# Performance work log

Measured on AMD Instinct MI355X. Metric: run time of the kernel, lower is better.

## Reference

```python
import jax, jax.numpy as jnp
import numpy as np

N = 500000
TOL = 0.01
ALPHA = 0.1
SLOPE = 0.01
EPS = 1e-10


def smooth_relu(x):
    # 0 for x<0; x^2/2 for 0<=x<1; x-1/2 for x>=1 (C1 smooth ReLU)
    return jnp.where(x < 0, 0.0, jnp.where(x < 1, 0.5 * x * x, x - 0.5))


def leaky_relu(x):
    return jnp.where(x >= 0, x, SLOPE * x)


def _xavier(key, shape):
    fan_out, fan_in = shape
    std = np.sqrt(2.0 / (fan_in + fan_out)).astype(np.float32)
    return jax.random.normal(key, shape, dtype=jnp.float32) * std


def setup_inputs() -> dict:
    key = jax.random.key(0)
    ks = jax.random.split(key, 16)
    inp = {
        'X': jax.random.normal(ks[0], (N, 2), dtype=jnp.float32),
        'Xstable': jnp.zeros((N, 2), dtype=jnp.float32),
        'Vl1_w': _xavier(ks[1], (64, 2)),
        'V2x_w': _xavier(ks[2], (64, 2)),
        'V2z_w': _xavier(ks[3], (64, 64)),
        'V3x_w': _xavier(ks[4], (64, 2)),
        'V3z_w': _xavier(ks[5], (64, 64)),
        'Vfx_w': _xavier(ks[6], (1, 2)),
        'Vfz_w': _xavier(ks[7], (1, 64)),
        'f1_w': _xavier(ks[8], (128, 2)),
        'f1_b': jnp.zeros((128,), dtype=jnp.float32),
        'f2_w': _xavier(ks[9], (128, 128)),
        'f2_b': jnp.zeros((128,), dtype=jnp.float32),
        'f3_w': _xavier(ks[10], (128, 128)),
        'f3_b': jnp.zeros((128,), dtype=jnp.float32),
        'f4_w': _xavier(ks[11], (128, 128)),
        'f4_b': jnp.zeros((128,), dtype=jnp.float32),
        'f5_w': _xavier(ks[12], (128, 128)),
        'f5_b': jnp.zeros((128,), dtype=jnp.float32),
        'ff_w': _xavier(ks[13], (2, 128)),
        'ff_b': jnp.zeros((2,), dtype=jnp.float32),
    }
    return inp


def _V_forward(X, Xstable, Vl1_w, V2x_w, V2z_w, V3x_w, V3z_w, Vfx_w, Vfz_w):
    d = X - Xstable                                  # [N,2]
    z1 = smooth_relu(d @ Vl1_w.T)                    # [N,64]
    z2 = smooth_relu(d @ V2x_w.T + z1 @ V2z_w.T)     # [N,64]
    z3 = smooth_relu(d @ V3x_w.T + z2 @ V3z_w.T)     # [N,64]
    zf = smooth_relu(d @ Vfx_w.T + z3 @ Vfz_w.T)     # [N,1]
    vsum = TOL * jnp.sum(d * d, axis=1, keepdims=True)
    return smooth_relu(zf) + vsum                    # [N,1]


def _fhat_forward(X, f1_w, f1_b, f2_w, f2_b, f3_w, f3_b, f4_w, f4_b, f5_w, f5_b, ff_w, ff_b):
    h = leaky_relu(X @ f1_w.T + f1_b)
    h = leaky_relu(h @ f2_w.T + f2_b)
    h = leaky_relu(h @ f3_w.T + f3_b)
    h = leaky_relu(h @ f4_w.T + f4_b)
    h = leaky_relu(h @ f5_w.T + f5_b)
    return h @ ff_w.T + ff_b                         # [N,2]


def reference(X, Xstable, Vl1_w, V2x_w, V2z_w, V3x_w, V3z_w, Vfx_w, Vfz_w,
              f1_w, f1_b, f2_w, f2_b, f3_w, f3_b, f4_w, f4_b, f5_w, f5_b, ff_w, ff_b):
    def Vfn(Xv):
        return _V_forward(Xv, Xstable, Vl1_w, V2x_w, V2z_w, V3x_w, V3z_w, Vfx_w, Vfz_w)

    V, pullback = jax.vjp(Vfn, X)
    gradV = pullback(jnp.ones_like(V))[0]            # dV/dX, [N,2]

    f_hat = _fhat_forward(X, f1_w, f1_b, f2_w, f2_b, f3_w, f3_b,
                          f4_w, f4_b, f5_w, f5_b, ff_w, ff_b)

    Vnorm = jnp.sum(gradV * gradV, axis=1, keepdims=True)      # [N,1]
    fh_V = jnp.sum(f_hat * gradV, axis=1, keepdims=True)       # [N,1]
    f_mul = jax.nn.relu(fh_V + ALPHA * V) / (Vnorm + EPS)      # [N,1]
    f = f_hat - gradV * f_mul                                  # [N,2]
    return f
```

## Files before the change

### kernel.cpp

```cpp
#include <hip/hip_runtime.h>


typedef _Float16 v2h __attribute__((ext_vector_type(2)));
typedef __fp16   v2hf __attribute__((ext_vector_type(2)));
typedef _Float16 v4h __attribute__((ext_vector_type(4)));
typedef _Float16 v8h __attribute__((ext_vector_type(8)));
typedef float    v4f __attribute__((ext_vector_type(4)));

__device__ __forceinline__ v2h cvt_pk(float a, float b){
  v2hf r = __builtin_amdgcn_cvt_pkrtz(a, b);
  union { v2hf f; v2h h; } u; u.f = r;
  return u.h;
}

#define NPTS 500000
#define FUSED_GRID ((NPTS + 255) / 256)

#define BAR_LDS() asm volatile("s_waitcnt lgkmcnt(0)\n\ts_barrier" ::: "memory")

#define OFF_FW    0
#define OFF_V2Z   65536
#define OFF_V3Z   69632
#define OFF_V2ZT  73728
#define OFF_V3ZT  77824
#define OFF_VL1T  81920
#define OFF_V2XT  82048
#define OFF_V3XT  82176
#define OFF_VFZ   82304
#define OFF_FFW   82368
#define OFF_F1W   82624
#define OFF_F1P   82880
#define OFF_V2XP  86976
#define OFF_V3XP  89024
#define W16_DATA  91072
#define W16_TOTAL (W16_DATA + 2048)

__device__ __align__(16) _Float16 g_w16[W16_TOTAL];

__device__ __forceinline__ float srelu(float x){
  float c = fminf(fmaxf(x, 0.f), 1.f);
  return c * fmaf(-0.5f, c, x);
}
__device__ __forceinline__ float sreluD(float x){
  return fminf(fmaxf(x, 0.f), 1.f);
}
__device__ __forceinline__ float sreluD_from_z(float z){
  return fminf(sqrtf(2.f * z), 1.f);
}

__device__ __forceinline__ v2h lrelu_pk(float a, float b){
  v2h x = cvt_pk(a, b);
  v2h m = x * (v2h){(_Float16)0.01f, (_Float16)0.01f};
  return __builtin_elementwise_max(x, m);
}
__device__ __forceinline__ v2h srelu_pk(float a, float b){
  v2h x = cvt_pk(a, b);
  const v2h z0 = (v2h){(_Float16)0.f, (_Float16)0.f};
  const v2h o1 = (v2h){(_Float16)1.f, (_Float16)1.f};
  const v2h hf = (v2h){(_Float16)0.5f, (_Float16)0.5f};
  v2h c = __builtin_elementwise_min(__builtin_elementwise_max(x, z0), o1);
  v2h t = x - c * hf;
  return c * t;
}

__global__ __launch_bounds__(256) void prep_kernel(
  const float* __restrict__ f2w, const float* __restrict__ f3w,
  const float* __restrict__ f4w, const float* __restrict__ f5w,
  const float* __restrict__ V2z, const float* __restrict__ V3z,
  const float* __restrict__ Vl1, const float* __restrict__ V2x,
  const float* __restrict__ V3x, const float* __restrict__ Vfz,
  const float* __restrict__ ffw, const float* __restrict__ f1w)
{
  const int i = blockIdx.x * 256 + threadIdx.x;
  if (i >= W16_TOTAL) return;
  if (i >= W16_DATA){ g_w16[i] = (_Float16)0.f; return; }
  float v;
  if (i < 65536){
    const float* W[4] = {f2w, f3w, f4w, f5w};
    v = W[i >> 14][i & 16383];
  } else if (i < 69632)  v = V2z[i - 65536];
  else if (i < 73728)    v = V3z[i - 69632];
  else if (i < 77824){ int r = i - 73728; v = V2z[(r & 63)*64 + (r >> 6)]; }
  else if (i < 81920){ int r = i - 77824; v = V3z[(r & 63)*64 + (r >> 6)]; }
  else if (i < 82048){ int r = i - 81920; v = Vl1[(r & 63)*2 + (r >> 6)]; }
  else if (i < 82176){ int r = i - 82048; v = V2x[(r & 63)*2 + (r >> 6)]; }
  else if (i < 82304){ int r = i - 82176; v = V3x[(r & 63)*2 + (r >> 6)]; }
  else if (i < 82368)    v = Vfz[i - 82304];
  else if (i < 82624)    v = ffw[i - 82368];
  else if (i < 82880)    v = f1w[i - 82624];
  else if (i < 86976){ int r = i - 82880; int k = r & 31; v = (k < 2) ? f1w[(r >> 5)*2 + k] : 0.f; }
  else if (i < 89024){ int r = i - 86976; int k = r & 31; v = (k < 2) ? V2x[(r >> 5)*2 + k] : 0.f; }
  else               { int r = i - 89024; int k = r & 31; v = (k < 2) ? V3x[(r >> 5)*2 + k] : 0.f; }
  g_w16[i] = (_Float16)v;
}

__device__ __forceinline__ void fh_layer(_Float16* H,
    const _Float16* __restrict__ Wl, const float* __restrict__ Bp,
    int w, int lm, int q)
{
  const v4f bv = *(const v4f*)(Bp + w*16 + q*4);
  v4f acc[16];
#pragma unroll
  for (int nt = 0; nt < 16; ++nt) acc[nt] = bv;

#pragma unroll
  for (int kt = 0; kt < 4; ++kt){
    const int sw = ((kt*4 + q) ^ lm) << 3;
    v8h A = *(const v8h*)(Wl + (w*16 + lm)*128 + kt*32 + q*8);
#pragma unroll
    for (int nt = 0; nt < 16; ++nt){
      v8h B = *(const v8h*)(H + (nt*16 + lm)*128 + sw);
      acc[nt] = __builtin_amdgcn_mfma_f32_16x16x32_f16(A, B, acc[nt], 0,0,0);
    }
  }
  BAR_LDS();
  const int o0 = w*16 + q*4;
  const int coff = (((o0 >> 3) ^ lm) << 3) + (o0 & 7);
#pragma unroll
  for (int nt = 0; nt < 16; ++nt){
    v4h hv;
    *(v2h*)&hv       = lrelu_pk(acc[nt][0], acc[nt][1]);
    *((v2h*)&hv + 1) = lrelu_pk(acc[nt][2], acc[nt][3]);
    *(v4h*)(H + (nt*16 + lm)*128 + coff) = hv;
  }
  BAR_LDS();
}

__device__ __forceinline__ void vfwd2_l2(_Float16* zoutA, _Float16* zoutB,
    const _Float16* __restrict__ Wz,
    const _Float16* __restrict__ WxP,
    const _Float16* __restrict__ Wl1T,
    v8h BdA, v8h BdB,
    float dA0, float dA1, float dB0, float dB1,
    float* __restrict__ sdA, float* __restrict__ sdB,
    int lm, int q)
{
  v4f accA[4], accB[4];
#pragma unroll
  for (int mt = 0; mt < 4; ++mt){
    accA[mt] = (v4f){0.f,0.f,0.f,0.f};
    accB[mt] = (v4f){0.f,0.f,0.f,0.f};
  }
  const int rs = lm & 7;
#pragma unroll
  for (int mt = 0; mt < 4; ++mt){
    v8h Ax = *(const v8h*)(WxP + (mt*16 + lm)*32 + q*8);
    accA[mt] = __builtin_amdgcn_mfma_f32_16x16x32_f16(Ax, BdA, accA[mt], 0,0,0);
    accB[mt] = __builtin_amdgcn_mfma_f32_16x16x32_f16(Ax, BdB, accB[mt], 0,0,0);
  }
#pragma unroll
  for (int kt = 0; kt < 2; ++kt){
    v8h w0 = *(const v8h*)(Wl1T + kt*32 + q*8);
    v8h w1 = *(const v8h*)(Wl1T + 64 + kt*32 + q*8);
    v8h BA, BB;
#pragma unroll
    for (int j2 = 0; j2 < 4; ++j2){
      const float a0 = (float)w0[2*j2  ], a1 = (float)w0[2*j2+1];
      const float c0 = (float)w1[2*j2  ], c1 = (float)w1[2*j2+1];
      ((v2h*)&BA)[j2] = srelu_pk(fmaf(dA0,a0,dA1*c0), fmaf(dA0,a1,dA1*c1));
      ((v2h*)&BB)[j2] = srelu_pk(fmaf(dB0,a0,dB1*c0), fmaf(dB0,a1,dB1*c1));
    }
#pragma unroll
    for (int mt = 0; mt < 4; ++mt){
      v8h A = *(const v8h*)(Wz + (mt*16 + lm)*64 + kt*32 + q*8);
      accA[mt] = __builtin_amdgcn_mfma_f32_16x16x32_f16(A, BA, accA[mt], 0,0,0);
      accB[mt] = __builtin_amdgcn_mfma_f32_16x16x32_f16(A, BB, accB[mt], 0,0,0);
    }
  }
#pragma unroll
  for (int mt = 0; mt < 4; ++mt){
    const int o0 = mt*16 + q*4;
    const int off = (((o0 >> 3) ^ rs) << 3) + (o0 & 7);
#pragma unroll
    for (int reg = 0; reg < 4; ++reg){
      sdA[mt*4 + reg] = sreluD(accA[mt][reg]);
      sdB[mt*4 + reg] = sreluD(accB[mt][reg]);
    }
    v4h hA, hB;
    *(v2h*)&hA       = srelu_pk(accA[mt][0], accA[mt][1]);
    *((v2h*)&hA + 1) = srelu_pk(accA[mt][2], accA[mt][3]);
    *(v2h*)&hB       = srelu_pk(accB[mt][0], accB[mt][1]);
    *((v2h*)&hB + 1) = srelu_pk(accB[mt][2], accB[mt][3]);
    *(v4h*)(zoutA + lm*64 + off) = hA;
    *(v4h*)(zoutB + lm*64 + off) = hB;
  }
}

__device__ __forceinline__ void vfwd2(const _Float16* zinA, _Float16* zoutA,
    const _Float16* zinB, _Float16* zoutB,
    const _Float16* __restrict__ Wz,
    const _Float16* __restrict__ WxP,
    v8h BdA, v8h BdB, int lm, int q)
{
  v4f accA[4], accB[4];
#pragma unroll
  for (int mt = 0; mt < 4; ++mt){
    accA[mt] = (v4f){0.f,0.f,0.f,0.f};
    accB[mt] = (v4f){0.f,0.f,0.f,0.f};
  }
  const int rs = lm & 7;
#pragma unroll
  for (int mt = 0; mt < 4; ++mt){
    v8h Ax = *(const v8h*)(WxP + (mt*16 + lm)*32 + q*8);
    accA[mt] = __builtin_amdgcn_mfma_f32_16x16x32_f16(Ax, BdA, accA[mt], 0,0,0);
    accB[mt] = __builtin_amdgcn_mfma_f32_16x16x32_f16(Ax, BdB, accB[mt], 0,0,0);
  }
#pragma unroll
  for (int kt = 0; kt < 2; ++kt){
    const int sw = (((kt*4 + q) ^ rs) << 3);
    v8h BA = *(const v8h*)(zinA + lm*64 + sw);
    v8h BB = *(const v8h*)(zinB + lm*64 + sw);
#pragma unroll
    for (int mt = 0; mt < 4; ++mt){
      v8h A = *(const v8h*)(Wz + (mt*16 + lm)*64 + kt*32 + q*8);
      accA[mt] = __builtin_amdgcn_mfma_f32_16x16x32_f16(A, BA, accA[mt], 0,0,0);
      accB[mt] = __builtin_amdgcn_mfma_f32_16x16x32_f16(A, BB, accB[mt], 0,0,0);
    }
  }
#pragma unroll
  for (int mt = 0; mt < 4; ++mt){
    const int o0 = mt*16 + q*4;
    const int off = (((o0 >> 3) ^ rs) << 3) + (o0 & 7);
    v4h hA, hB;
    *(v2h*)&hA       = srelu_pk(accA[mt][0], accA[mt][1]);
    *((v2h*)&hA + 1) = srelu_pk(accA[mt][2], accA[mt][3]);
    *(v2h*)&hB       = srelu_pk(accB[mt][0], accB[mt][1]);
    *((v2h*)&hB + 1) = srelu_pk(accB[mt][2], accB[mt][3]);
    *(v4h*)(zoutA + lm*64 + off) = hA;
    *(v4h*)(zoutB + lm*64 + off) = hB;
  }
}

__device__ __forceinline__ void vbwd2(const _Float16* ginA, _Float16* zioA,
    const _Float16* ginB, _Float16* zioB,
    const _Float16* __restrict__ WT,
    const float* __restrict__ sdA, const float* __restrict__ sdB,
    int lm, int q)
{
  v4f accA[4], accB[4];
#pragma unroll
  for (int mt = 0; mt < 4; ++mt){
    accA[mt] = (v4f){0.f,0.f,0.f,0.f};
    accB[mt] = (v4f){0.f,0.f,0.f,0.f};
  }
  const int rs = lm & 7;
#pragma unroll
  for (int kt = 0; kt < 2; ++kt){
    const int sw = (((kt*4 + q) ^ rs) << 3);
    v8h BA = *(const v8h*)(ginA + lm*64 + sw);
    v8h BB = *(const v8h*)(ginB + lm*64 + sw);
#pragma unroll
    for (int mt = 0; mt < 4; ++mt){
      v8h A = *(const v8h*)(WT + (mt*16 + lm)*64 + kt*32 + q*8);
      accA[mt] = __builtin_amdgcn_mfma_f32_16x16x32_f16(A, BA, accA[mt], 0,0,0);
      accB[mt] = __builtin_amdgcn_mfma_f32_16x16x32_f16(A, BB, accB[mt], 0,0,0);
    }
  }
#pragma unroll
  for (int mt = 0; mt < 4; ++mt){
    const int k0 = mt*16 + q*4;
    const int off = (((k0 >> 3) ^ rs) << 3) + (k0 & 7);
    v4h gA, gB;
    *(v2h*)&gA       = cvt_pk(accA[mt][0]*sdA[mt*4+0], accA[mt][1]*sdA[mt*4+1]);
    *((v2h*)&gA + 1) = cvt_pk(accA[mt][2]*sdA[mt*4+2], accA[mt][3]*sdA[mt*4+3]);
    *(v2h*)&gB       = cvt_pk(accB[mt][0]*sdB[mt*4+0], accB[mt][1]*sdB[mt*4+1]);
    *((v2h*)&gB + 1) = cvt_pk(accB[mt][2]*sdB[mt*4+2], accB[mt][3]*sdB[mt*4+3]);
    *(v4h*)(zioA + lm*64 + off) = gA;
    *(v4h*)(zioB + lm*64 + off) = gB;
  }
}

__device__ __forceinline__ void vbwd2_l1(_Float16* zioA, _Float16* zioB,
    const _Float16* __restrict__ WT,
    const _Float16* __restrict__ Wl1T,
    float dA0, float dA1, float dB0, float dB1, int lm, int q)
{
  v4f accA[4], accB[4];
#pragma unroll
  for (int mt = 0; mt < 4; ++mt){
    accA[mt] = (v4f){0.f,0.f,0.f,0.f};
    accB[mt] = (v4f){0.f,0.f,0.f,0.f};
  }
  const int rs = lm & 7;
#pragma unroll
  for (int kt = 0; kt < 2; ++kt){
    const int sw = (((kt*4 + q) ^ rs) << 3);
    v8h BA = *(const v8h*)(zioA + lm*64 + sw);
    v8h BB = *(const v8h*)(zioB + lm*64 + sw);
#pragma unroll
    for (int mt = 0; mt < 4; ++mt){
      v8h A = *(const v8h*)(WT + (mt*16 + lm)*64 + kt*32 + q*8);
      accA[mt] = __builtin_amdgcn_mfma_f32_16x16x32_f16(A, BA, accA[mt], 0,0,0);
      accB[mt] = __builtin_amdgcn_mfma_f32_16x16x32_f16(A, BB, accB[mt], 0,0,0);
    }
  }
#pragma unroll
  for (int mt = 0; mt < 4; ++mt){
    const int k0 = mt*16 + q*4;
    const int off = (((k0 >> 3) ^ rs) << 3) + (k0 & 7);
    v4h w0 = *(const v4h*)(Wl1T + k0);
    v4h w1 = *(const v4h*)(Wl1T + 64 + k0);
    float sA[4], sB[4];
#pragma unroll
    for (int reg = 0; reg < 4; ++reg){
      const float a1A = fmaf(dA0, (float)w0[reg], dA1 * (float)w1[reg]);
      const float a1B = fmaf(dB0, (float)w0[reg], dB1 * (float)w1[reg]);
      sA[reg] = accA[mt][reg] * sreluD(a1A);
      sB[reg] = accB[mt][reg] * sreluD(a1B);
    }
    v4h gA, gB;
    *(v2h*)&gA       = cvt_pk(sA[0], sA[1]);
    *((v2h*)&gA + 1) = cvt_pk(sA[2], sA[3]);
    *(v2h*)&gB       = cvt_pk(sB[0], sB[1]);
    *((v2h*)&gB + 1) = cvt_pk(sB[2], sB[3]);
    *(v4h*)(zioA + lm*64 + off) = gA;
    *(v4h*)(zioB + lm*64 + off) = gB;
  }
}

__device__ __forceinline__ void gacc2(v4f& aGA, v4f& aGB,
    const _Float16* __restrict__ WxTbase,
    const _Float16* ZA, const _Float16* ZB, int lm, int q)
{
  const int rs = lm & 7;
#pragma unroll
  for (int kt = 0; kt < 2; ++kt){
    const int sw = (((kt*4 + q) ^ rs) << 3);
    v8h A  = *(const v8h*)(WxTbase + lm*64 + kt*32 + q*8);
    v8h BA = *(const v8h*)(ZA + lm*64 + sw);
    v8h BB = *(const v8h*)(ZB + lm*64 + sw);
    aGA = __builtin_amdgcn_mfma_f32_16x16x32_f16(A, BA, aGA, 0,0,0);
    aGB = __builtin_amdgcn_mfma_f32_16x16x32_f16(A, BB, aGB, 0,0,0);
  }
}

__global__ __launch_bounds__(512, 4) void fused_kernel(
  const float* __restrict__ X, const float* __restrict__ Xst,
  const float* __restrict__ Vfx,
  const float* __restrict__ f1b, const float* __restrict__ f2b,
  const float* __restrict__ f3b, const float* __restrict__ f4b,
  const float* __restrict__ f5b, const float* __restrict__ ffb,
  float* __restrict__ out)
{
  __shared__ __align__(16) char smem[65536];
  _Float16* const H = (_Float16*)smem;

  const int b  = blockIdx.x;
  const int t  = threadIdx.x;
  const int w  = t >> 6;
  const int l  = t & 63;
  const int lm = l & 15;
  const int q  = l >> 4;
  const int rs = lm & 7;
  const int row0 = b*256 + w*32;

  const int r0 = row0 + lm;
  const int r1 = row0 + 16 + lm;
  const int rc0 = r0 < NPTS ? r0 : NPTS-1;
  const int rc1 = r1 < NPTS ? r1 : NPTS-1;
  const float2 x0 = *(const float2*)(X + rc0*2);
  const float2 x1 = *(const float2*)(X + rc1*2);

  {
    v8h Bx0 = (v8h){(_Float16)0.f,(_Float16)0.f,(_Float16)0.f,(_Float16)0.f,
                    (_Float16)0.f,(_Float16)0.f,(_Float16)0.f,(_Float16)0.f};
    v8h Bx1 = Bx0;
    if (q == 0){
      Bx0[0] = (_Float16)x0.x; Bx0[1] = (_Float16)x0.y;
      Bx1[0] = (_Float16)x1.x; Bx1[1] = (_Float16)x1.y;
    }
#pragma unroll
    for (int mt = 0; mt < 8; ++mt){
      const int o0 = mt*16 + q*4;
      const v4f bv = *(const v4f*)(f1b + o0);
      v8h A = *(const v8h*)(g_w16 + OFF_F1P + (mt*16 + lm)*32 + q*8);
      v4f a0 = __builtin_amdgcn_mfma_f32_16x16x32_f16(A, Bx0, bv, 0,0,0);
      v4f a1 = __builtin_amdgcn_mfma_f32_16x16x32_f16(A, Bx1, bv, 0,0,0);
      const int coff = (((o0 >> 3) ^ lm) << 3) + (o0 & 7);
      v4h h0, h1;
      *(v2h*)&h0       = lrelu_pk(a0[0], a0[1]);
      *((v2h*)&h0 + 1) = lrelu_pk(a0[2], a0[3]);
      *(v2h*)&h1       = lrelu_pk(a1[0], a1[1]);
      *((v2h*)&h1 + 1) = lrelu_pk(a1[2], a1[3]);
      *(v4h*)(H + (w*32 + lm)*128 + coff)      = h0;
      *(v4h*)(H + (w*32 + 16 + lm)*128 + coff) = h1;
    }
  }
  BAR_LDS();

  fh_layer(H, g_w16 + OFF_FW,         f2b, w, lm, q);
  fh_layer(H, g_w16 + OFF_FW + 16384, f3b, w, lm, q);
  fh_layer(H, g_w16 + OFF_FW + 32768, f4b, w, lm, q);
  fh_layer(H, g_w16 + OFF_FW + 49152, f5b, w, lm, q);

  float fhA0, fhA1, fhB0, fhB1;
  {
    v4f a0 = (v4f){0.f,0.f,0.f,0.f};
    v4f a1 = (v4f){0.f,0.f,0.f,0.f};
#pragma unroll
    for (int kt = 0; kt < 4; ++kt){
      const int sw = ((kt*4 + q) ^ lm) << 3;
      v8h A  = *(const v8h*)(g_w16 + OFF_FFW + lm*128 + kt*32 + q*8);
      v8h B0 = *(const v8h*)(H + (w*32 + lm)*128 + sw);
      v8h B1 = *(const v8h*)(H + (w*32 + 16 + lm)*128 + sw);
      a0 = __builtin_amdgcn_mfma_f32_16x16x32_f16(A, B0, a0, 0,0,0);
      a1 = __builtin_amdgcn_mfma_f32_16x16x32_f16(A, B1, a1, 0,0,0);
    }
    const float fb0 = ffb[0], fb1 = ffb[1];
    fhA0 = a0[0] + fb0; fhA1 = a0[1] + fb1;
    fhB0 = a1[0] + fb0; fhB1 = a1[1] + fb1;
  }

  _Float16* const ZA2 = (_Float16*)(smem + w*8192);
  _Float16* const ZA3 = ZA2 + 1024;
  _Float16* const ZB2 = ZA2 + 2048;
  _Float16* const ZB3 = ZA2 + 3072;

  const float2 sA = *(const float2*)(Xst + rc0*2);
  const float2 sB = *(const float2*)(Xst + rc1*2);
  const float dA0 = x0.x - sA.x, dA1 = x0.y - sA.y;
  const float dB0 = x1.x - sB.x, dB1 = x1.y - sB.y;
  const float vfx0 = Vfx[0], vfx1 = Vfx[1];

  v8h BdA = (v8h){(_Float16)0.f,(_Float16)0.f,(_Float16)0.f,(_Float16)0.f,
                  (_Float16)0.f,(_Float16)0.f,(_Float16)0.f,(_Float16)0.f};
  v8h BdB = BdA;
  if (q == 0){
    BdA[0] = (_Float16)dA0; BdA[1] = (_Float16)dA1;
    BdB[0] = (_Float16)dB0; BdB[1] = (_Float16)dB1;
  }

  float sdA2[16], sdB2[16];
  vfwd2_l2(ZA2, ZB2, g_w16 + OFF_V2Z, g_w16 + OFF_V2XP, g_w16 + OFF_VL1T,
           BdA, BdB, dA0, dA1, dB0, dB1, sdA2, sdB2, lm, q);
  vfwd2(ZA2, ZA3, ZB2, ZB3, g_w16 + OFF_V3Z, g_w16 + OFF_V3XP,
        BdA, BdB, lm, q);

  float VVrA, sfA, VVrB, sfB;
  {
    v4f aSA = (v4f){0.f,0.f,0.f,0.f};
    v4f aSB = (v4f){0.f,0.f,0.f,0.f};
#pragma unroll
    for (int kt = 0; kt < 2; ++kt){
      const int sw = (((kt*4 + q) ^ rs) << 3);
      v8h A  = *(const v8h*)(g_w16 + OFF_VFZ + lm*64 + kt*32 + q*8);
      v8h BA = *(const v8h*)(ZA3 + lm*64 + sw);
      v8h BB = *(const v8h*)(ZB3 + lm*64 + sw);
      aSA = __builtin_amdgcn_mfma_f32_16x16x32_f16(A, BA, aSA, 0,0,0);
      aSB = __builtin_amdgcn_mfma_f32_16x16x32_f16(A, BB, aSB, 0,0,0);
    }
    const float afA = fmaf(vfx0, dA0, fmaf(vfx1, dA1, aSA[0]));
    const float zfA = srelu(afA);
    VVrA = srelu(zfA) + 0.01f * fmaf(dA0, dA0, dA1*dA1);
    sfA  = sreluD(zfA) * sreluD(afA);
    const float afB = fmaf(vfx0, dB0, fmaf(vfx1, dB1, aSB[0]));
    const float zfB = srelu(afB);
    VVrB = srelu(zfB) + 0.01f * fmaf(dB0, dB0, dB1*dB1);
    sfB  = sreluD(zfB) * sreluD(afB);
  }

#pragma unroll
  for (int cc = 0; cc < 2; ++cc){
    const int c = q*2 + cc;
    const int sw = ((c ^ rs) << 3);
    v8h vf = *(const v8h*)(g_w16 + OFF_VFZ + c*8);
    _Float16* pA = ZA3 + lm*64 + sw;
    _Float16* pB = ZB3 + lm*64 + sw;
    v8h zA = *(const v8h*)pA;
    v8h zB = *(const v8h*)pB;
    v8h uA, uB;
#pragma unroll
    for (int j2 = 0; j2 < 4; ++j2){
      float a0 = (float)vf[2*j2  ] * sreluD_from_z((float)zA[2*j2  ]);
      float a1 = (float)vf[2*j2+1] * sreluD_from_z((float)zA[2*j2+1]);
      float b0 = (float)vf[2*j2  ] * sreluD_from_z((float)zB[2*j2  ]);
      float b1 = (float)vf[2*j2+1] * sreluD_from_z((float)zB[2*j2+1]);
      ((v2h*)&uA)[j2] = cvt_pk(a0, a1);
      ((v2h*)&uB)[j2] = cvt_pk(b0, b1);
    }
    *(v8h*)pA = uA;
    *(v8h*)pB = uB;
  }

  v4f aGA = (v4f){0.f,0.f,0.f,0.f};
  v4f aGB = (v4f){0.f,0.f,0.f,0.f};

  gacc2(aGA, aGB, g_w16 + OFF_V3XT, ZA3, ZB3, lm, q);
  vbwd2(ZA3, ZA2, ZB3, ZB2, g_w16 + OFF_V3ZT, sdA2, sdB2, lm, q);
  gacc2(aGA, aGB, g_w16 + OFF_V2XT, ZA2, ZB2, lm, q);
  vbwd2_l1(ZA2, ZB2, g_w16 + OFF_V2ZT, g_w16 + OFF_VL1T,
           dA0, dA1, dB0, dB1, lm, q);
  gacc2(aGA, aGB, g_w16 + OFF_VL1T, ZA2, ZB2, lm, q);

  const float g0A = fmaf(0.02f, dA0, sfA * (vfx0 + aGA[0]));
  const float g1A = fmaf(0.02f, dA1, sfA * (vfx1 + aGA[1]));
  const float g0B = fmaf(0.02f, dB0, sfB * (vfx0 + aGB[0]));
  const float g1B = fmaf(0.02f, dB1, sfB * (vfx1 + aGB[1]));

  if (q == 0){
    if (r0 < NPTS){
      const float Vn  = fmaf(g0A, g0A, g1A*g1A);
      const float num = fmaf(0.1f, VVrA, fmaf(fhA0, g0A, fhA1*g1A));
      const float fm  = fmaxf(num, 0.f) / (Vn + 1e-10f);
      *(float2*)(out + r0*2) =
        make_float2(fmaf(-g0A, fm, fhA0), fmaf(-g1A, fm, fhA1));
    }
    if (r1 < NPTS){
      const float Vn  = fmaf(g0B, g0B, g1B*g1B);
      const float num = fmaf(0.1f, VVrB, fmaf(fhB0, g0B, fhB1*g1B));
      const float fm  = fmaxf(num, 0.f) / (Vn + 1e-10f);
      *(float2*)(out + r1*2) =
        make_float2(fmaf(-g0B, fm, fhB0), fmaf(-g1B, fm, fhB1));
    }
  }
}

extern "C" void kernel_launch(void* const* d_in, const int* in_sizes, int n_in,
                              void* d_out, int out_size, void* d_ws, size_t ws_size,
                              hipStream_t stream)
{
  (void)d_ws; (void)ws_size; (void)n_in; (void)in_sizes; (void)out_size;
  const float* X   = (const float*)d_in[0];
  const float* Xst = (const float*)d_in[1];
  const float* Vl1 = (const float*)d_in[2];
  const float* V2x = (const float*)d_in[3];
  const float* V2z = (const float*)d_in[4];
  const float* V3x = (const float*)d_in[5];
  const float* V3z = (const float*)d_in[6];
  const float* Vfx = (const float*)d_in[7];
  const float* Vfz = (const float*)d_in[8];
  const float* f1w = (const float*)d_in[9];
  const float* f1b = (const float*)d_in[10];
  const float* f2w = (const float*)d_in[11];
  const float* f2b = (const float*)d_in[12];
  const float* f3w = (const float*)d_in[13];
  const float* f3b = (const float*)d_in[14];
  const float* f4w = (const float*)d_in[15];
  const float* f4b = (const float*)d_in[16];
  const float* f5w = (const float*)d_in[17];
  const float* f5b = (const float*)d_in[18];
  const float* ffw = (const float*)d_in[19];
  const float* ffb = (const float*)d_in[20];

  prep_kernel<<<(W16_TOTAL + 255)/256, 256, 0, stream>>>(
      f2w, f3w, f4w, f5w, V2z, V3z, Vl1, V2x, V3x, Vfz, ffw, f1w);
  fused_kernel<<<FUSED_GRID, 512, 0, stream>>>(
      X, Xst, Vfx, f1b, f2b, f3b, f4b, f5b, ffb, (float*)d_out);
}
```

Baseline: 254.3 us.

## Use 32x32x16 MFMA for f-hat hidden layers and keep layer-3 srelu derivatives in registers

The four 128x128 f-hat layers move from 16x16x32 MFMA tiles (16 per wave) to 32x32x16 tiles: each wave now computes a 32-feature by 128-row block, with a new LDS swizzle for reading and writing. This means fewer A-fragment loads and fewer MFMA issues per output. Separately, the layer-3 V smooth-ReLU derivative is saved in registers during the forward pass, replacing the later step that rebuilt it from stored fp16 activations with a sqrt. Both changes raise register use (v16f accumulators, 32 extra floats), which may lower occupancy.

```diff
diff --git a/kernel.cpp b/kernel.cpp
--- a/kernel.cpp
+++ b/kernel.cpp
@@ -6,6 +6,7 @@
 typedef _Float16 v4h __attribute__((ext_vector_type(4)));
 typedef _Float16 v8h __attribute__((ext_vector_type(8)));
 typedef float    v4f __attribute__((ext_vector_type(4)));
+typedef float    v16f __attribute__((ext_vector_type(16)));
 
 __device__ __forceinline__ v2h cvt_pk(float a, float b){
   v2hf r = __builtin_amdgcn_cvt_pkrtz(a, b);
@@ -43,9 +44,6 @@
 }
 __device__ __forceinline__ float sreluD(float x){
   return fminf(fmaxf(x, 0.f), 1.f);
-}
-__device__ __forceinline__ float sreluD_from_z(float z){
-  return fminf(sqrtf(2.f * z), 1.f);
 }
 
 __device__ __forceinline__ v2h lrelu_pk(float a, float b){
@@ -94,35 +92,57 @@
   g_w16[i] = (_Float16)v;
 }
 
-__device__ __forceinline__ void fh_layer(_Float16* H,
+__device__ __forceinline__ void fh_layer32(_Float16* H,
     const _Float16* __restrict__ Wl, const float* __restrict__ Bp,
-    int w, int lm, int q)
-{
-  const v4f bv = *(const v4f*)(Bp + w*16 + q*4);
-  v4f acc[16];
-#pragma unroll
-  for (int nt = 0; nt < 16; ++nt) acc[nt] = bv;
-
-#pragma unroll
-  for (int kt = 0; kt < 4; ++kt){
-    const int sw = ((kt*4 + q) ^ lm) << 3;
-    v8h A = *(const v8h*)(Wl + (w*16 + lm)*128 + kt*32 + q*8);
-#pragma unroll
-    for (int nt = 0; nt < 16; ++nt){
-      v8h B = *(const v8h*)(H + (nt*16 + lm)*128 + sw);
-      acc[nt] = __builtin_amdgcn_mfma_f32_16x16x32_f16(A, B, acc[nt], 0,0,0);
-    }
+    int fw, int rh, int l)
+{
+  const int ar = l & 31;
+  const int kg = l >> 5;
+
+  v16f bias;
+#pragma unroll
+  for (int tq = 0; tq < 4; ++tq){
+    const v4f bq = *(const v4f*)(Bp + fw*32 + 8*tq + 4*kg);
+    bias[tq*4+0] = bq[0]; bias[tq*4+1] = bq[1];
+    bias[tq*4+2] = bq[2]; bias[tq*4+3] = bq[3];
+  }
+  v16f acc0 = bias, acc1 = bias, acc2 = bias, acc3 = bias;
+
+  const int r0  = rh*128 + ar;
+  const int rsw = r0 & 15;
+  const _Float16* wp = Wl + (fw*32 + ar)*128 + kg*8;
+  const _Float16* hp = H + r0*128;
+
+#pragma unroll
+  for (int kt = 0; kt < 8; ++kt){
+    v8h A = *(const v8h*)(wp + kt*16);
+    const int sw = ((kt*2 + kg) ^ rsw) << 3;
+    v8h B0 = *(const v8h*)(hp            + sw);
+    v8h B1 = *(const v8h*)(hp + 32*128   + sw);
+    v8h B2 = *(const v8h*)(hp + 64*128   + sw);
+    v8h B3 = *(const v8h*)(hp + 96*128   + sw);
+    acc0 = __builtin_amdgcn_mfma_f32_32x32x16_f16(A, B0, acc0, 0,0,0);
+    acc1 = __builtin_amdgcn_mfma_f32_32x32x16_f16(A, B1, acc1, 0,0,0);
+    acc2 = __builtin_amdgcn_mfma_f32_32x32x16_f16(A, B2, acc2, 0,0,0);
+    acc3 = __builtin_amdgcn_mfma_f32_32x32x16_f16(A, B3, acc3, 0,0,0);
   }
   BAR_LDS();
-  const int o0 = w*16 + q*4;
-  const int coff = (((o0 >> 3) ^ lm) << 3) + (o0 & 7);
-#pragma unroll
-  for (int nt = 0; nt < 16; ++nt){
-    v4h hv;
-    *(v2h*)&hv       = lrelu_pk(acc[nt][0], acc[nt][1]);
-    *((v2h*)&hv + 1) = lrelu_pk(acc[nt][2], acc[nt][3]);
-    *(v4h*)(H + (nt*16 + lm)*128 + coff) = hv;
-  }
+
+#define FH_EPI32(ACC, NTOFF) { \
+  _Float16* op = H + (r0 + NTOFF)*128; \
+  _Pragma("unroll") \
+  for (int tq = 0; tq < 4; ++tq){ \
+    const int coff = (((fw*4 + tq) ^ rsw) << 3) + 4*kg; \
+    v4h hv; \
+    *(v2h*)&hv       = lrelu_pk(ACC[tq*4+0], ACC[tq*4+1]); \
+    *((v2h*)&hv + 1) = lrelu_pk(ACC[tq*4+2], ACC[tq*4+3]); \
+    *(v4h*)(op + coff) = hv; \
+  } }
+  FH_EPI32(acc0, 0)
+  FH_EPI32(acc1, 32)
+  FH_EPI32(acc2, 64)
+  FH_EPI32(acc3, 96)
+#undef FH_EPI32
   BAR_LDS();
 }
 
@@ -190,7 +210,9 @@
     const _Float16* zinB, _Float16* zoutB,
     const _Float16* __restrict__ Wz,
     const _Float16* __restrict__ WxP,
-    v8h BdA, v8h BdB, int lm, int q)
+    v8h BdA, v8h BdB,
+    float* __restrict__ sdA, float* __restrict__ sdB,
+    int lm, int q)
 {
   v4f accA[4], accB[4];
 #pragma unroll
@@ -221,6 +243,11 @@
   for (int mt = 0; mt < 4; ++mt){
     const int o0 = mt*16 + q*4;
     const int off = (((o0 >> 3) ^ rs) << 3) + (o0 & 7);
+#pragma unroll
+    for (int reg = 0; reg < 4; ++reg){
+      sdA[mt*4 + reg] = sreluD(accA[mt][reg]);
+      sdB[mt*4 + reg] = sreluD(accB[mt][reg]);
+    }
     v4h hA, hB;
     *(v2h*)&hA       = srelu_pk(accA[mt][0], accA[mt][1]);
     *((v2h*)&hA + 1) = srelu_pk(accA[mt][2], accA[mt][3]);
@@ -388,10 +415,14 @@
   }
   BAR_LDS();
 
-  fh_layer(H, g_w16 + OFF_FW,         f2b, w, lm, q);
-  fh_layer(H, g_w16 + OFF_FW + 16384, f3b, w, lm, q);
-  fh_layer(H, g_w16 + OFF_FW + 32768, f4b, w, lm, q);
-  fh_layer(H, g_w16 + OFF_FW + 49152, f5b, w, lm, q);
+  {
+    const int fw = w & 3;
+    const int rh = w >> 2;
+    fh_layer32(H, g_w16 + OFF_FW,         f2b, fw, rh, l);
+    fh_layer32(H, g_w16 + OFF_FW + 16384, f3b, fw, rh, l);
+    fh_layer32(H, g_w16 + OFF_FW + 32768, f4b, fw, rh, l);
+    fh_layer32(H, g_w16 + OFF_FW + 49152, f5b, fw, rh, l);
+  }
 
   float fhA0, fhA1, fhB0, fhB1;
   {
@@ -430,11 +461,11 @@
     BdB[0] = (_Float16)dB0; BdB[1] = (_Float16)dB1;
   }
 
-  float sdA2[16], sdB2[16];
+  float sdA2[16], sdB2[16], sdA3[16], sdB3[16];
   vfwd2_l2(ZA2, ZB2, g_w16 + OFF_V2Z, g_w16 + OFF_V2XP, g_w16 + OFF_VL1T,
            BdA, BdB, dA0, dA1, dB0, dB1, sdA2, sdB2, lm, q);
   vfwd2(ZA2, ZA3, ZB2, ZB3, g_w16 + OFF_V3Z, g_w16 + OFF_V3XP,
-        BdA, BdB, lm, q);
+        BdA, BdB, sdA3, sdB3, lm, q);
 
   float VVrA, sfA, VVrB, sfB;
   {
@@ -460,26 +491,17 @@
   }
 
 #pragma unroll
-  for (int cc = 0; cc < 2; ++cc){
-    const int c = q*2 + cc;
-    const int sw = ((c ^ rs) << 3);
-    v8h vf = *(const v8h*)(g_w16 + OFF_VFZ + c*8);
-    _Float16* pA = ZA3 + lm*64 + sw;
-    _Float16* pB = ZB3 + lm*64 + sw;
-    v8h zA = *(const v8h*)pA;
-    v8h zB = *(const v8h*)pB;
-    v8h uA, uB;
-#pragma unroll
-    for (int j2 = 0; j2 < 4; ++j2){
-      float a0 = (float)vf[2*j2  ] * sreluD_from_z((float)zA[2*j2  ]);
-      float a1 = (float)vf[2*j2+1] * sreluD_from_z((float)zA[2*j2+1]);
-      float b0 = (float)vf[2*j2  ] * sreluD_from_z((float)zB[2*j2  ]);
-      float b1 = (float)vf[2*j2+1] * sreluD_from_z((float)zB[2*j2+1]);
-      ((v2h*)&uA)[j2] = cvt_pk(a0, a1);
-      ((v2h*)&uB)[j2] = cvt_pk(b0, b1);
-    }
-    *(v8h*)pA = uA;
-    *(v8h*)pB = uB;
+  for (int mt = 0; mt < 4; ++mt){
+    const int o0 = mt*16 + q*4;
+    const int off = (((o0 >> 3) ^ rs) << 3) + (o0 & 7);
+    const v4h vfq = *(const v4h*)(g_w16 + OFF_VFZ + o0);
+    v4h uA, uB;
+    *(v2h*)&uA       = cvt_pk((float)vfq[0]*sdA3[mt*4+0], (float)vfq[1]*sdA3[mt*4+1]);
+    *((v2h*)&uA + 1) = cvt_pk((float)vfq[2]*sdA3[mt*4+2], (float)vfq[3]*sdA3[mt*4+3]);
+    *(v2h*)&uB       = cvt_pk((float)vfq[0]*sdB3[mt*4+0], (float)vfq[1]*sdB3[mt*4+1]);
+    *((v2h*)&uB + 1) = cvt_pk((float)vfq[2]*sdB3[mt*4+2], (float)vfq[3]*sdB3[mt*4+3]);
+    *(v4h*)(ZA3 + lm*64 + off) = uA;
+    *(v4h*)(ZB3 + lm*64 + off) = uB;
   }
 
   v4f aGA = (v4f){0.f,0.f,0.f,0.f};
```

Measured after the change: 280.7 us. 1.1x slower.
